# Kernel tuning notes

Measured on AMD Instinct MI355X. Metric: run time of the kernel, lower is better.

Reference implementation:

```python
import jax, jax.numpy as jnp
import numpy as np

B = 131072
N_EMBD = 512
PRED_LEN = 8
HID = 66   # 64 + 1 (light) + 1 (cmd)
INP = 16   # 2 (x) + 2 (tp) + 2 (x_last) + 10 (box)


def setup_inputs() -> dict:
    key = jax.random.key(0)
    ks = jax.random.split(key, 14)
    s = 0.1  # small param scale
    return {
        "x_last": jax.random.normal(ks[0], (B, PRED_LEN, 2), jnp.float32),
        "cls_emb": jax.random.normal(ks[1], (B, N_EMBD), jnp.float32),
        "tp_batch": jax.random.normal(ks[2], (B, 2), jnp.float32),
        "light_batch": jax.random.normal(ks[3], (B, 1), jnp.float32),
        "cmd_batch": jax.random.normal(ks[4], (B, 1), jnp.float32),
        "batch_npred_bbox": jax.random.normal(ks[5], (B, 1, PRED_LEN, 10), jnp.float32),
        "W_head": jax.random.normal(ks[6], (64, N_EMBD), jnp.float32) * s,
        "b_head": jax.random.normal(ks[7], (64,), jnp.float32) * s,
        "W_ih": jax.random.normal(ks[8], (3 * HID, INP), jnp.float32) * s,
        "W_hh": jax.random.normal(ks[9], (3 * HID, HID), jnp.float32) * s,
        "b_ih": jax.random.normal(ks[10], (3 * HID,), jnp.float32) * s,
        "b_hh": jax.random.normal(ks[11], (3 * HID,), jnp.float32) * s,
        "W_out": jax.random.normal(ks[12], (2, HID), jnp.float32) * s,
        "b_out": jax.random.normal(ks[13], (2,), jnp.float32) * s,
    }


def reference(x_last, cls_emb, tp_batch, light_batch, cmd_batch, batch_npred_bbox,
              W_head, b_head, W_ih, W_hh, b_ih, b_hh, W_out, b_out):
    bs = cls_emb.shape[0]
    # initial hidden state: wp_head(cls_emb) ++ light ++ cmd  -> [B, 66]
    z0 = jnp.concatenate([cls_emb @ W_head.T + b_head, light_batch, cmd_batch], axis=1)
    x0 = jnp.zeros((bs, 2), dtype=cls_emb.dtype)

    # per-step inputs: [T, B, 2] and [T, B, 10]
    xl_steps = jnp.moveaxis(x_last, 1, 0)
    bb_steps = jnp.moveaxis(batch_npred_bbox, 2, 0).reshape(PRED_LEN, bs, -1)

    def gru_cell(x_in, h):
        gi = x_in @ W_ih.T + b_ih            # [B, 3H]
        gh = h @ W_hh.T + b_hh               # [B, 3H]
        r = jax.nn.sigmoid(gi[:, :HID] + gh[:, :HID])
        u = jax.nn.sigmoid(gi[:, HID:2 * HID] + gh[:, HID:2 * HID])
        n = jnp.tanh(gi[:, 2 * HID:] + r * gh[:, 2 * HID:])
        return (1.0 - u) * n + u * h

    def step(carry, inp):
        z, x = carry
        xl, bb = inp
        x_in = jnp.concatenate([x, tp_batch, xl, bb], axis=1)  # [B, 16]
        z = gru_cell(x_in, z)
        x = z @ W_out.T + b_out + x
        return (z, x), x

    _, wps = jax.lax.scan(step, (z0, x0), (xl_steps, bb_steps))  # [T, B, 2]
    pred_wp = jnp.moveaxis(wps, 0, 1)  # [B, T, 2]
    # pred_wp[:, :, 0] -= 1.3
    pred_wp = pred_wp - jnp.array([1.3, 0.0], dtype=pred_wp.dtype)
    return pred_wp
```

## Files before the change

### kernel.cpp

```cpp
#include <hip/hip_runtime.h>

#define N_EMBD 512
#define HID 66
#define T_STEPS 8
#define BLK 128

__device__ __forceinline__ float fast_rcp(float a) {
    float r = __builtin_amdgcn_rcpf(a);
    r = r * (2.0f - a * r);
    return r;
}
__device__ __forceinline__ float fast_exp(float x) {
    x = fminf(x, 60.0f);
    return __expf(x);
}
__device__ __forceinline__ float sigmoid_f(float x) {
    return fast_rcp(1.0f + fast_exp(-x));
}
__device__ __forceinline__ float tanh_f(float x) {
    return 1.0f - 2.0f * fast_rcp(1.0f + fast_exp(2.0f * x));
}

__global__ __launch_bounds__(BLK, 2) void wp_grurefine_kernel(
    const float* __restrict__ x_last,
    const float* __restrict__ cls_emb,
    const float* __restrict__ tp,
    const float* __restrict__ light,
    const float* __restrict__ cmd,
    const float* __restrict__ bbox,
    const float* __restrict__ W_head,
    const float* __restrict__ b_head,
    const float* __restrict__ W_ih,
    const float* __restrict__ W_hh,
    const float* __restrict__ b_ih,
    const float* __restrict__ b_hh,
    const float* __restrict__ W_out,
    const float* __restrict__ b_out,
    float* __restrict__ out,
    int Btotal)
{
    __shared__ float h_lds[BLK][HID];
    const int tl = threadIdx.x;
    const int b  = blockIdx.x * BLK + tl;
    if (b >= Btotal) return;

    float h[HID];
    #pragma unroll
    for (int j = 0; j < 64; ++j) h[j] = b_head[j];

    const float* cls = cls_emb + (size_t)b * N_EMBD;
    #pragma unroll 1
    for (int k0 = 0; k0 < N_EMBD; k0 += 4) {
        const float4 c = *(const float4*)(cls + k0);
        #pragma unroll
        for (int j = 0; j < 64; ++j) {
            const float* wr = W_head + j * N_EMBD + k0;
            h[j] = fmaf(c.x, wr[0],
                   fmaf(c.y, wr[1],
                   fmaf(c.z, wr[2],
                   fmaf(c.w, wr[3], h[j]))));
        }
    }
    h[64] = light[b];
    h[65] = cmd[b];

    #pragma unroll
    for (int j = 0; j < HID; ++j) h_lds[tl][j] = h[j];

    const float tp0 = tp[(size_t)b * 2 + 0];
    const float tp1 = tp[(size_t)b * 2 + 1];
    const float* xlr = x_last + (size_t)b * (T_STEPS * 2);
    const float* bbr = bbox   + (size_t)b * (T_STEPS * 10);
    float*       outr = out   + (size_t)b * (T_STEPS * 2);

    float x0 = 0.0f, x1 = 0.0f;

    #pragma unroll 1
    for (int t = 0; t < T_STEPS; ++t) {
        float xin[16];
        xin[0] = x0;  xin[1] = x1;
        xin[2] = tp0; xin[3] = tp1;
        xin[4] = xlr[t * 2 + 0];
        xin[5] = xlr[t * 2 + 1];
        #pragma unroll
        for (int q = 0; q < 10; ++q) xin[6 + q] = bbr[t * 10 + q];

        #pragma unroll 1
        for (int j = 0; j < HID; ++j) {
            const float* wir = W_ih + j * 16;
            const float* wiu = W_ih + (HID + j) * 16;
            const float* win = W_ih + (2 * HID + j) * 16;
            const float* whr = W_hh + j * HID;
            const float* whu = W_hh + (HID + j) * HID;
            const float* whn = W_hh + (2 * HID + j) * HID;

            float gr  = b_ih[j]           + b_hh[j];
            float gu  = b_ih[HID + j]     + b_hh[HID + j];
            float gin = b_ih[2 * HID + j];
            float ghn = b_hh[2 * HID + j];

            #pragma unroll
            for (int k = 0; k < 16; ++k) {
                gr  = fmaf(xin[k], wir[k], gr);
                gu  = fmaf(xin[k], wiu[k], gu);
                gin = fmaf(xin[k], win[k], gin);
            }
            #pragma unroll
            for (int k = 0; k < HID; ++k) {
                gr  = fmaf(h[k], whr[k], gr);
                gu  = fmaf(h[k], whu[k], gu);
                ghn = fmaf(h[k], whn[k], ghn);
            }

            const float r = sigmoid_f(gr);
            const float u = sigmoid_f(gu);
            const float n = tanh_f(fmaf(r, ghn, gin));
            const float hold = h_lds[tl][j];
            h_lds[tl][j] = (1.0f - u) * n + u * hold;
        }

        float a0 = b_out[0], a1 = b_out[1];
        #pragma unroll
        for (int j = 0; j < HID; ++j) {
            const float z = h_lds[tl][j];
            h[j] = z;
            a0 = fmaf(z, W_out[j],       a0);
            a1 = fmaf(z, W_out[HID + j], a1);
        }
        x0 += a0;
        x1 += a1;

        outr[t * 2 + 0] = x0 - 1.3f;
        outr[t * 2 + 1] = x1;
    }
}

extern "C" void kernel_launch(void* const* d_in, const int* in_sizes, int n_in,
                              void* d_out, int out_size, void* d_ws, size_t ws_size,
                              hipStream_t stream) {
    const float* x_last  = (const float*)d_in[0];
    const float* cls_emb = (const float*)d_in[1];
    const float* tp      = (const float*)d_in[2];
    const float* light   = (const float*)d_in[3];
    const float* cmd     = (const float*)d_in[4];
    const float* bbox    = (const float*)d_in[5];
    const float* W_head  = (const float*)d_in[6];
    const float* b_head  = (const float*)d_in[7];
    const float* W_ih    = (const float*)d_in[8];
    const float* W_hh    = (const float*)d_in[9];
    const float* b_ih    = (const float*)d_in[10];
    const float* b_hh    = (const float*)d_in[11];
    const float* W_out   = (const float*)d_in[12];
    const float* b_out   = (const float*)d_in[13];
    float* out = (float*)d_out;

    const int Btotal = in_sizes[1] / N_EMBD;
    dim3 grid((Btotal + BLK - 1) / BLK);
    wp_grurefine_kernel<<<grid, BLK, 0, stream>>>(
        x_last, cls_emb, tp, light, cmd, bbox,
        W_head, b_head, W_ih, W_hh, b_ih, b_hh, W_out, b_out,
        out, Btotal);
}
```

Measured before the change: 2.340 ms.

## Keep GRU hidden state in registers, fully unroll gate loop, shrink block

Removes the LDS scratch buffer for the hidden state. A second register array now holds the new hidden values, and the 66-iteration gate loop is fully unrolled so the array can be indexed statically. The block size drops to 64, the head GEMV loop is widened to 8 elements per iteration, and per-step inputs are loaded as float2 vectors. This removes LDS traffic and gives the compiler scheduling freedom, at the cost of a much larger unrolled body, roughly 132+ live registers per thread, lower occupancy and possible spills.

Result: slower. 3.082 ms (+31.7%).

```diff
diff --git a/kernel.cpp b/kernel.cpp
--- a/kernel.cpp
+++ b/kernel.cpp
@@ -3,7 +3,7 @@
 #define N_EMBD 512
 #define HID 66
 #define T_STEPS 8
-#define BLK 128
+#define BLK 64
 
 __device__ __forceinline__ float fast_rcp(float a) {
     float r = __builtin_amdgcn_rcpf(a);
@@ -39,9 +39,7 @@
     float* __restrict__ out,
     int Btotal)
 {
-    __shared__ float h_lds[BLK][HID];
-    const int tl = threadIdx.x;
-    const int b  = blockIdx.x * BLK + tl;
+    const int b = blockIdx.x * BLK + threadIdx.x;
     if (b >= Btotal) return;
 
     float h[HID];
@@ -50,28 +48,32 @@
 
     const float* cls = cls_emb + (size_t)b * N_EMBD;
     #pragma unroll 1
-    for (int k0 = 0; k0 < N_EMBD; k0 += 4) {
-        const float4 c = *(const float4*)(cls + k0);
+    for (int k0 = 0; k0 < N_EMBD; k0 += 8) {
+        const float4 c0 = *(const float4*)(cls + k0);
+        const float4 c1 = *(const float4*)(cls + k0 + 4);
         #pragma unroll
         for (int j = 0; j < 64; ++j) {
             const float* wr = W_head + j * N_EMBD + k0;
-            h[j] = fmaf(c.x, wr[0],
-                   fmaf(c.y, wr[1],
-                   fmaf(c.z, wr[2],
-                   fmaf(c.w, wr[3], h[j]))));
+            float acc = h[j];
+            acc = fmaf(c0.x, wr[0], acc);
+            acc = fmaf(c0.y, wr[1], acc);
+            acc = fmaf(c0.z, wr[2], acc);
+            acc = fmaf(c0.w, wr[3], acc);
+            acc = fmaf(c1.x, wr[4], acc);
+            acc = fmaf(c1.y, wr[5], acc);
+            acc = fmaf(c1.z, wr[6], acc);
+            acc = fmaf(c1.w, wr[7], acc);
+            h[j] = acc;
         }
     }
     h[64] = light[b];
     h[65] = cmd[b];
 
-    #pragma unroll
-    for (int j = 0; j < HID; ++j) h_lds[tl][j] = h[j];
-
-    const float tp0 = tp[(size_t)b * 2 + 0];
-    const float tp1 = tp[(size_t)b * 2 + 1];
-    const float* xlr = x_last + (size_t)b * (T_STEPS * 2);
-    const float* bbr = bbox   + (size_t)b * (T_STEPS * 10);
-    float*       outr = out   + (size_t)b * (T_STEPS * 2);
+    const float2 tpv = *(const float2*)(tp + (size_t)b * 2);
+    const float tp0 = tpv.x, tp1 = tpv.y;
+    const float* xlr  = x_last + (size_t)b * (T_STEPS * 2);
+    const float* bbr  = bbox   + (size_t)b * (T_STEPS * 10);
+    float*       outr = out    + (size_t)b * (T_STEPS * 2);
 
     float x0 = 0.0f, x1 = 0.0f;
 
@@ -80,12 +82,19 @@
         float xin[16];
         xin[0] = x0;  xin[1] = x1;
         xin[2] = tp0; xin[3] = tp1;
-        xin[4] = xlr[t * 2 + 0];
-        xin[5] = xlr[t * 2 + 1];
+        {
+            const float2 xl2 = *(const float2*)(xlr + t * 2);
+            xin[4] = xl2.x; xin[5] = xl2.y;
+        }
         #pragma unroll
-        for (int q = 0; q < 10; ++q) xin[6 + q] = bbr[t * 10 + q];
+        for (int q = 0; q < 5; ++q) {
+            const float2 bq = *(const float2*)(bbr + t * 10 + q * 2);
+            xin[6 + 2 * q] = bq.x;
+            xin[7 + 2 * q] = bq.y;
+        }
 
-        #pragma unroll 1
+        float hn[HID];
+        #pragma unroll
         for (int j = 0; j < HID; ++j) {
             const float* wir = W_ih + j * 16;
             const float* wiu = W_ih + (HID + j) * 16;
@@ -115,14 +124,13 @@
             const float r = sigmoid_f(gr);
             const float u = sigmoid_f(gu);
             const float n = tanh_f(fmaf(r, ghn, gin));
-            const float hold = h_lds[tl][j];
-            h_lds[tl][j] = (1.0f - u) * n + u * hold;
+            hn[j] = (1.0f - u) * n + u * h[j];
         }
 
         float a0 = b_out[0], a1 = b_out[1];
         #pragma unroll
         for (int j = 0; j < HID; ++j) {
-            const float z = h_lds[tl][j];
+            const float z = hn[j];
             h[j] = z;
             a0 = fmaf(z, W_out[j],       a0);
             a1 = fmaf(z, W_out[HID + j], a1);
```
